# Kernel tuning notes

Measured on AMD Instinct MI355X. Metric: run time of the kernel, lower is better.

The kernel has to match this reference:

```python
import jax, jax.numpy as jnp
import numpy as np

B, T, D, H = 2, 2048, 1024, 16
DK = D // H


def setup_inputs() -> dict:
    key = jax.random.key(0)
    ks = jax.random.split(key, 9)
    x = jax.random.normal(ks[0], (B, T, D), dtype=jnp.float32)
    # causal mask, broadcastable to [B, H, T, T]; positions with 0 are masked
    mask = jnp.tril(jnp.ones((T, T), dtype=jnp.int32))[None, None]
    s = 1.0 / np.sqrt(D)
    Wq = jax.random.normal(ks[1], (D, D), dtype=jnp.float32) * s
    Wk = jax.random.normal(ks[2], (D, D), dtype=jnp.float32) * s
    Wv = jax.random.normal(ks[3], (D, D), dtype=jnp.float32) * s
    Wo = jax.random.normal(ks[4], (D, D), dtype=jnp.float32) * s
    bq = jnp.zeros((D,), jnp.float32)
    bk = jnp.zeros((D,), jnp.float32)
    bv = jnp.zeros((D,), jnp.float32)
    bo = jnp.zeros((D,), jnp.float32)
    return {"x": x, "mask": mask, "Wq": Wq, "bq": bq, "Wk": Wk, "bk": bk,
            "Wv": Wv, "bv": bv, "Wo": Wo, "bo": bo}


def _split_heads(t):
    # [B, T, D] -> [B, H, T, DK]
    return t.reshape(B, T, H, DK).transpose(0, 2, 1, 3)


def reference(x, mask, Wq, bq, Wk, bk, Wv, bv, Wo, bo):
    Q = _split_heads(x @ Wq.T + bq)
    K = _split_heads(x @ Wk.T + bk)
    V = _split_heads(x @ Wv.T + bv)
    scores = jnp.einsum('bhqd,bhkd->bhqk', Q, K) / jnp.sqrt(jnp.float32(DK))
    scores = jnp.where(mask == 0, jnp.float32(-1e9), scores)
    attn = jax.nn.softmax(scores, axis=-1)  # dropout p=0 -> identity
    out = jnp.einsum('bhqk,bhkd->bhqd', attn, V)
    out = out.transpose(0, 2, 1, 3).reshape(B, T, D)
    out = out @ Wo.T + bo
    return (out, attn)
```

## Files before the change

### kernel.cpp

```cpp
#include <hip/hip_runtime.h>
#include <hip/hip_bf16.h>
#include <cstdint>


typedef __attribute__((ext_vector_type(8))) short bf16x8;
typedef __attribute__((ext_vector_type(4))) float f32x4;

#define MFMA(a,b,c) __builtin_amdgcn_mfma_f32_16x16x32_bf16((a),(b),(c),0,0,0)

static __device__ __forceinline__ short f2bf(float f) {
  __hip_bfloat16 h = __float2bfloat16(f);
  return (short)__builtin_bit_cast(ushort, h);
}

static __device__ __forceinline__ bf16x8 cvt8(const float* p) {
  float4 v0 = *(const float4*)p;
  float4 v1 = *(const float4*)(p + 4);
  bf16x8 r;
  r[0] = f2bf(v0.x); r[1] = f2bf(v0.y); r[2] = f2bf(v0.z); r[3] = f2bf(v0.w);
  r[4] = f2bf(v1.x); r[5] = f2bf(v1.y); r[6] = f2bf(v1.z); r[7] = f2bf(v1.w);
  return r;
}

__global__ __launch_bounds__(256)
void cvt_x(const float* __restrict__ x, ushort* __restrict__ xbf)
{
  const size_t i = ((size_t)blockIdx.x * 256 + threadIdx.x) * 8;
  const bf16x8 v = cvt8(x + i);
  *(bf16x8*)&xbf[i] = v;
}

__global__ __launch_bounds__(256)
void gemm_qkv(const ushort* __restrict__ Xbf,
              const float* __restrict__ Wq, const float* __restrict__ Wk,
              const float* __restrict__ Wv,
              const float* __restrict__ bq, const float* __restrict__ bk,
              const float* __restrict__ bv,
              ushort* __restrict__ Qw, ushort* __restrict__ Kw, ushort* __restrict__ Vt)
{
  __shared__ __align__(16) ushort As[128 * 32];
  __shared__ __align__(16) ushort Bs[128 * 32];
  const int tid  = threadIdx.x;
  const int lane = tid & 63;
  const int wid  = tid >> 6;
  const int wr = wid >> 1, wc = wid & 1;
  const int g = lane >> 4, c16 = lane & 15;
  const int i0 = blockIdx.x * 128;
  const int j0 = blockIdx.y * 128;

  const int widx = j0 >> 10;
  const int jj0  = j0 & 1023;
  const float* W    = (widx == 0) ? Wq : ((widx == 1) ? Wk : Wv);
  const float* bias = (widx == 0) ? bq : ((widx == 1) ? bk : bv);

  const int arow = tid >> 2;
  const int acol = (tid & 3) * 8;
  const ushort* a0p = Xbf + (size_t)(i0 + arow) * 1024 + acol;
  const ushort* a1p = a0p + (size_t)64 * 1024;
  const float*  b0p = W + (size_t)(jj0 + arow) * 1024 + acol;
  const float*  b1p = b0p + (size_t)64 * 1024;

  f32x4 acc[4][4];
#pragma unroll
  for (int mi = 0; mi < 4; ++mi)
#pragma unroll
    for (int ni = 0; ni < 4; ++ni) acc[mi][ni] = (f32x4){0.f, 0.f, 0.f, 0.f};

  for (int k0 = 0; k0 < 1024; k0 += 32) {
    const bf16x8 va0 = *(const bf16x8*)(a0p + k0);
    const bf16x8 va1 = *(const bf16x8*)(a1p + k0);
    const bf16x8 vb0 = cvt8(b0p + k0);
    const bf16x8 vb1 = cvt8(b1p + k0);
    __syncthreads();
    *(bf16x8*)&As[tid * 8]        = va0;
    *(bf16x8*)&As[2048 + tid * 8] = va1;
    *(bf16x8*)&Bs[tid * 8]        = vb0;
    *(bf16x8*)&Bs[2048 + tid * 8] = vb1;
    __syncthreads();
    bf16x8 af[4], bfv[4];
#pragma unroll
    for (int mi = 0; mi < 4; ++mi)
      af[mi] = *(const bf16x8*)&As[(wr * 64 + mi * 16 + c16) * 32 + g * 8];
#pragma unroll
    for (int ni = 0; ni < 4; ++ni)
      bfv[ni] = *(const bf16x8*)&Bs[(wc * 64 + ni * 16 + c16) * 32 + g * 8];
#pragma unroll
    for (int mi = 0; mi < 4; ++mi)
#pragma unroll
      for (int ni = 0; ni < 4; ++ni)
        acc[mi][ni] = MFMA(af[mi], bfv[ni], acc[mi][ni]);
  }

  float bv4[4];
#pragma unroll
  for (int ni = 0; ni < 4; ++ni) bv4[ni] = bias[jj0 + wc * 64 + ni * 16 + c16];

  if (widx < 2) {
    ushort* OP = (widx == 0) ? Qw : Kw;
#pragma unroll
    for (int mi = 0; mi < 4; ++mi) {
      const int ib = i0 + wr * 64 + mi * 16 + g * 4;
      const int b = ib >> 11, t = ib & 2047;
#pragma unroll
      for (int ni = 0; ni < 4; ++ni) {
        const int jj = jj0 + wc * 64 + ni * 16 + c16;
        const int h = jj >> 6, dk = jj & 63;
        const size_t base = ((size_t)(b * 16 + h) * 2048 + t) * 64 + dk;
#pragma unroll
        for (int r = 0; r < 4; ++r)
          OP[base + (size_t)r * 64] = (ushort)f2bf(acc[mi][ni][r] + bv4[ni]);
      }
    }
  } else {
#pragma unroll
    for (int mi = 0; mi < 4; ++mi) {
      const int ib = i0 + wr * 64 + mi * 16 + g * 4;
      const int b = ib >> 11, t = ib & 2047;
#pragma unroll
      for (int ni = 0; ni < 4; ++ni) {
        const int jj = jj0 + wc * 64 + ni * 16 + c16;
        ushort4 pk;
        pk.x = (ushort)f2bf(acc[mi][ni][0] + bv4[ni]);
        pk.y = (ushort)f2bf(acc[mi][ni][1] + bv4[ni]);
        pk.z = (ushort)f2bf(acc[mi][ni][2] + bv4[ni]);
        pk.w = (ushort)f2bf(acc[mi][ni][3] + bv4[ni]);
        *(ushort4*)&Vt[((size_t)b * 1024 + jj) * 2048 + t] = pk;
      }
    }
  }
}

__global__ __launch_bounds__(256)
void gemm_out(const ushort* __restrict__ ctx, const float* __restrict__ Wo,
              const float* __restrict__ bo, float* __restrict__ out)
{
  __shared__ __align__(16) ushort As[128 * 32];
  __shared__ __align__(16) ushort Bs[128 * 32];
  const int tid  = threadIdx.x;
  const int lane = tid & 63;
  const int wid  = tid >> 6;
  const int wr = wid >> 1, wc = wid & 1;
  const int g = lane >> 4, c16 = lane & 15;
  const int i0 = blockIdx.x * 128;
  const int j0 = blockIdx.y * 128;

  const int arow = tid >> 2;
  const int acol = (tid & 3) * 8;
  const ushort* a0p = ctx + (size_t)(i0 + arow) * 1024 + acol;
  const ushort* a1p = a0p + (size_t)64 * 1024;
  const float*  b0p = Wo + (size_t)(j0 + arow) * 1024 + acol;
  const float*  b1p = b0p + (size_t)64 * 1024;

  f32x4 acc[4][4];
#pragma unroll
  for (int mi = 0; mi < 4; ++mi)
#pragma unroll
    for (int ni = 0; ni < 4; ++ni) acc[mi][ni] = (f32x4){0.f, 0.f, 0.f, 0.f};

  for (int k0 = 0; k0 < 1024; k0 += 32) {
    const bf16x8 va0 = *(const bf16x8*)(a0p + k0);
    const bf16x8 va1 = *(const bf16x8*)(a1p + k0);
    const bf16x8 vb0 = cvt8(b0p + k0);
    const bf16x8 vb1 = cvt8(b1p + k0);
    __syncthreads();
    *(bf16x8*)&As[tid * 8]        = va0;
    *(bf16x8*)&As[2048 + tid * 8] = va1;
    *(bf16x8*)&Bs[tid * 8]        = vb0;
    *(bf16x8*)&Bs[2048 + tid * 8] = vb1;
    __syncthreads();
    bf16x8 af[4], bfv[4];
#pragma unroll
    for (int mi = 0; mi < 4; ++mi)
      af[mi] = *(const bf16x8*)&As[(wr * 64 + mi * 16 + c16) * 32 + g * 8];
#pragma unroll
    for (int ni = 0; ni < 4; ++ni)
      bfv[ni] = *(const bf16x8*)&Bs[(wc * 64 + ni * 16 + c16) * 32 + g * 8];
#pragma unroll
    for (int mi = 0; mi < 4; ++mi)
#pragma unroll
      for (int ni = 0; ni < 4; ++ni)
        acc[mi][ni] = MFMA(af[mi], bfv[ni], acc[mi][ni]);
  }

  float bv4[4];
#pragma unroll
  for (int ni = 0; ni < 4; ++ni) bv4[ni] = bo[j0 + wc * 64 + ni * 16 + c16];

#pragma unroll
  for (int mi = 0; mi < 4; ++mi) {
    const int ib = i0 + wr * 64 + mi * 16 + g * 4;
#pragma unroll
    for (int ni = 0; ni < 4; ++ni) {
      const int jj = j0 + wc * 64 + ni * 16 + c16;
#pragma unroll
      for (int r = 0; r < 4; ++r)
        out[(size_t)(ib + r) * 1024 + jj] = acc[mi][ni][r] + bv4[ni];
    }
  }
}

__global__ __launch_bounds__(256)
void attn_stats(const ushort* __restrict__ Qw, const ushort* __restrict__ Kw,
                const ushort* __restrict__ Vt, ushort* __restrict__ ctx,
                float* __restrict__ Linv)
{
  __shared__ __align__(16) ushort Ks[2][64][68];
  __shared__ __align__(16) ushort Vs[2][64][68];
  __shared__ __align__(16) ushort Plds[4][16][68];
  const int tid = threadIdx.x, lane = tid & 63, wid = tid >> 6;
  const int g = lane >> 4, c16 = lane & 15;
  const int pr = blockIdx.x;
  const int bh = blockIdx.y;
  const int b = bh >> 4, h = bh & 15;

  const ushort* kbase = Kw + (size_t)bh * (2048 * 64);
  const ushort* vbase = Vt + ((size_t)b * 1024 + h * 64) * 2048;

  const int sr = tid >> 2;
  const int sc = (tid & 3) * 16;
  const ushort* kst = kbase + (size_t)sr * 64 + sc;
  const ushort* vst = vbase + (size_t)sr * 2048 + sc;

  int cur = 0;

#pragma unroll
  for (int part = 0; part < 2; ++part) {
    const int qtile = part ? (31 - pr) : pr;
    const int qt = qtile * 64 + wid * 16;
    const int q = qt + c16;
    const int nch = qtile + 1;

    const ushort* qp = Qw + ((size_t)bh * 2048 + q) * 64 + g * 8;
    const bf16x8 qf0 = *(const bf16x8*)qp;
    const bf16x8 qf1 = *(const bf16x8*)(qp + 32);

    f32x4 o[4];
#pragma unroll
    for (int dt = 0; dt < 4; ++dt) o[dt] = (f32x4){0.f, 0.f, 0.f, 0.f};
    float lsum = 0.f;

    {
      const bf16x8 k0 = *(const bf16x8*)kst;
      const bf16x8 k1 = *(const bf16x8*)(kst + 8);
      const bf16x8 v0 = *(const bf16x8*)vst;
      const bf16x8 v1 = *(const bf16x8*)(vst + 8);
      __syncthreads();
      *(bf16x8*)&Ks[cur][sr][sc]     = k0;
      *(bf16x8*)&Ks[cur][sr][sc + 8] = k1;
      *(bf16x8*)&Vs[cur][sr][sc]     = v0;
      *(bf16x8*)&Vs[cur][sr][sc + 8] = v1;
    }

    for (int c = 0; c < nch; ++c) {
      bf16x8 k0, k1, v0, v1;
      const bool pf = (c + 1 < nch);
      if (pf) {
        const int kt1 = (c + 1) * 64;
        k0 = *(const bf16x8*)(kst + (size_t)kt1 * 64);
        k1 = *(const bf16x8*)(kst + (size_t)kt1 * 64 + 8);
        v0 = *(const bf16x8*)(vst + kt1);
        v1 = *(const bf16x8*)(vst + kt1 + 8);
      }
      __syncthreads();

      const int kt = c * 64;
      f32x4 sv[4];
#pragma unroll
      for (int s = 0; s < 4; ++s) {
        const bf16x8 kf0 = *(const bf16x8*)&Ks[cur][s * 16 + c16][g * 8];
        const bf16x8 kf1 = *(const bf16x8*)&Ks[cur][s * 16 + c16][32 + g * 8];
        f32x4 t0 = (f32x4){0.f, 0.f, 0.f, 0.f};
        t0 = MFMA(kf0, qf0, t0);
        t0 = MFMA(kf1, qf1, t0);
        sv[s] = t0;
      }

      if (c + 1 == nch) {
#pragma unroll
        for (int s = 0; s < 4; ++s) {
          short pk[4];
#pragma unroll
          for (int r = 0; r < 4; ++r) {
            const int k = kt + s * 16 + g * 4 + r;
            const float p = (k > q) ? 0.f : __expf(sv[s][r] * 0.125f - 20.f);
            lsum += p;
            pk[r] = f2bf(p);
          }
          *(short4*)&Plds[wid][c16][s * 16 + g * 4] = *(short4*)pk;
        }
      } else {
#pragma unroll
        for (int s = 0; s < 4; ++s) {
          short pk[4];
#pragma unroll
          for (int r = 0; r < 4; ++r) {
            const float p = __expf(sv[s][r] * 0.125f - 20.f);
            lsum += p;
            pk[r] = f2bf(p);
          }
          *(short4*)&Plds[wid][c16][s * 16 + g * 4] = *(short4*)pk;
        }
      }

      {
        const bf16x8 pa0 = *(const bf16x8*)&Plds[wid][c16][g * 8];
#pragma unroll
        for (int dt = 0; dt < 4; ++dt) {
          const bf16x8 vf = *(const bf16x8*)&Vs[cur][dt * 16 + c16][g * 8];
          o[dt] = MFMA(pa0, vf, o[dt]);
        }
        const bf16x8 pa1 = *(const bf16x8*)&Plds[wid][c16][32 + g * 8];
#pragma unroll
        for (int dt = 0; dt < 4; ++dt) {
          const bf16x8 vf = *(const bf16x8*)&Vs[cur][dt * 16 + c16][32 + g * 8];
          o[dt] = MFMA(pa1, vf, o[dt]);
        }
      }

      if (pf) {
        *(bf16x8*)&Ks[cur ^ 1][sr][sc]     = k0;
        *(bf16x8*)&Ks[cur ^ 1][sr][sc + 8] = k1;
        *(bf16x8*)&Vs[cur ^ 1][sr][sc]     = v0;
        *(bf16x8*)&Vs[cur ^ 1][sr][sc + 8] = v1;
        cur ^= 1;
      }
    }

    lsum += __shfl_xor(lsum, 16);
    lsum += __shfl_xor(lsum, 32);
    const float linv = 1.f / lsum;
    if (g == 0) Linv[(size_t)bh * 2048 + q] = linv;

#pragma unroll
    for (int r = 0; r < 4; ++r) {
      const float lr = __shfl(linv, g * 4 + r);
#pragma unroll
      for (int dt = 0; dt < 4; ++dt)
        ctx[((size_t)(b * 2048 + qt + g * 4 + r)) * 1024 + h * 64 + dt * 16 + c16] =
            (ushort)f2bf(o[dt][r] * lr);
    }
  }
}

__global__ __launch_bounds__(256)
void attn_tiles(const ushort* __restrict__ Qw, const ushort* __restrict__ Kw,
                const float* __restrict__ Linv, float* __restrict__ attn)
{
  const int tid = threadIdx.x, lane = tid & 63, wid = tid >> 6;
  const int g = lane >> 4, c16 = lane & 15;
  const int bh = blockIdx.y;
  const int n = blockIdx.x * 4 + wid;
  int qtile = (int)((sqrtf(8.f * n + 1.f) - 1.f) * 0.5f);
  while ((qtile + 1) * (qtile + 2) / 2 <= n) ++qtile;
  while (qtile * (qtile + 1) / 2 > n) --qtile;
  const int ktile = n - qtile * (qtile + 1) / 2;
  const int qt0 = qtile * 64, kt0 = ktile * 64;
  float* abase = attn + ((size_t)bh * 2048) * 2048;

  const ushort* qbase = Qw + ((size_t)bh * 2048 + qt0) * 64;
  const ushort* kbase = Kw + ((size_t)bh * 2048 + kt0) * 64;
  bf16x8 qf0[4], qf1[4];
  float lv[4];
#pragma unroll
  for (int sq = 0; sq < 4; ++sq) {
    const ushort* qp = qbase + (size_t)(sq * 16 + c16) * 64 + g * 8;
    qf0[sq] = *(const bf16x8*)qp;
    qf1[sq] = *(const bf16x8*)(qp + 32);
    lv[sq] = Linv[(size_t)bh * 2048 + qt0 + sq * 16 + c16];
  }

  if (ktile < qtile) {
#pragma unroll
    for (int sk = 0; sk < 4; ++sk) {
      const ushort* kp = kbase + (size_t)(sk * 16 + c16) * 64 + g * 8;
      const bf16x8 kf0 = *(const bf16x8*)kp;
      const bf16x8 kf1 = *(const bf16x8*)(kp + 32);
#pragma unroll
      for (int sq = 0; sq < 4; ++sq) {
        f32x4 t = (f32x4){0.f, 0.f, 0.f, 0.f};
        t = MFMA(kf0, qf0[sq], t);
        t = MFMA(kf1, qf1[sq], t);
        const int qq = qt0 + sq * 16 + c16;
        f32x4 st;
#pragma unroll
        for (int r = 0; r < 4; ++r)
          st[r] = __expf(t[r] * 0.125f - 20.f) * lv[sq];
        __builtin_nontemporal_store(st,
            (f32x4*)(abase + (size_t)qq * 2048 + kt0 + sk * 16 + g * 4));
      }
    }
  } else {
#pragma unroll
    for (int sk = 0; sk < 4; ++sk) {
      const ushort* kp = kbase + (size_t)(sk * 16 + c16) * 64 + g * 8;
      const bf16x8 kf0 = *(const bf16x8*)kp;
      const bf16x8 kf1 = *(const bf16x8*)(kp + 32);
#pragma unroll
      for (int sq = 0; sq < 4; ++sq) {
        f32x4 t = (f32x4){0.f, 0.f, 0.f, 0.f};
        t = MFMA(kf0, qf0[sq], t);
        t = MFMA(kf1, qf1[sq], t);
        const int qq = qt0 + sq * 16 + c16;
        f32x4 st;
#pragma unroll
        for (int r = 0; r < 4; ++r) {
          const int kk = kt0 + sk * 16 + g * 4 + r;
          st[r] = (kk > qq) ? 0.f : __expf(t[r] * 0.125f - 20.f) * lv[sq];
        }
        __builtin_nontemporal_store(st,
            (f32x4*)(abase + (size_t)qq * 2048 + kt0 + sk * 16 + g * 4));
      }
    }
  }
}

__global__ __launch_bounds__(256)
void attn_zeros(float* __restrict__ attn)
{
  const int tid = threadIdx.x, lane = tid & 63, wid = tid >> 6;
  const int qtile = blockIdx.x;
  const int bh = blockIdx.y;
  const int zstart = (qtile + 1) * 64;
  const int zlen = 2048 - zstart;
  float* base = attn + ((size_t)bh * 2048 + qtile * 64) * 2048;
  const f32x4 z = (f32x4){0.f, 0.f, 0.f, 0.f};
#pragma unroll
  for (int rr = 0; rr < 16; ++rr) {
    float* rowp = base + (size_t)(wid * 16 + rr) * 2048 + zstart;
    for (int c = lane * 4; c < zlen; c += 256)
      __builtin_nontemporal_store(z, (f32x4*)(rowp + c));
  }
}

extern "C" void kernel_launch(void* const* d_in, const int* in_sizes, int n_in,
                              void* d_out, int out_size, void* d_ws, size_t ws_size,
                              hipStream_t stream)
{
  const float* x  = (const float*)d_in[0];
  const float* Wq = (const float*)d_in[2];
  const float* bq = (const float*)d_in[3];
  const float* Wk = (const float*)d_in[4];
  const float* bk = (const float*)d_in[5];
  const float* Wv = (const float*)d_in[6];
  const float* bv = (const float*)d_in[7];
  const float* Wo = (const float*)d_in[8];
  const float* bo = (const float*)d_in[9];

  if (ws_size < (size_t)33816576) return;

  float* out  = (float*)d_out;
  float* attn = out + (size_t)4194304;

  ushort* ws   = (ushort*)d_ws;
  ushort* Qw   = ws;
  ushort* Kw   = Qw + (size_t)4194304;
  ushort* Vtw  = Kw + (size_t)4194304;
  ushort* ctx  = Vtw + (size_t)4194304;
  float*  Linv = (float*)(ctx + (size_t)4194304);

  cvt_x<<<dim3(2048), 256, 0, stream>>>(x, ctx);
  gemm_qkv<<<dim3(32, 24), 256, 0, stream>>>(ctx, Wq, Wk, Wv, bq, bk, bv, Qw, Kw, Vtw);
  attn_stats<<<dim3(16, 32), 256, 0, stream>>>(Qw, Kw, Vtw, ctx, Linv);
  attn_zeros<<<dim3(31, 32), 256, 0, stream>>>(attn);
  attn_tiles<<<dim3(132, 32), 256, 0, stream>>>(Qw, Kw, Linv, attn);
  gemm_out<<<dim3(32, 8), 256, 0, stream>>>(ctx, Wo, bo, out);
}
```

Measured before the change: 272.3 us.

## Merge attention stats with zero-fill and attn tiles with output GEMM

Combines four launches into two by putting independent work into one grid. The attention-stats blocks and the upper-triangle zero-fill blocks share the first kernel. The probability-tile blocks and the output projection GEMM blocks share the second, each dispatched by blockIdx range. The aim is to cut launch overhead and let bandwidth-bound zero-fill and attn writes overlap with compute-bound work. The cost is heavier per-block register and LDS footprints, since each merged kernel takes the larger of its two roles, which may lower occupancy.

```diff
diff --git a/kernel.cpp b/kernel.cpp
--- a/kernel.cpp
+++ b/kernel.cpp
@@ -131,18 +131,250 @@
 }
 
 __global__ __launch_bounds__(256)
-void gemm_out(const ushort* __restrict__ ctx, const float* __restrict__ Wo,
-              const float* __restrict__ bo, float* __restrict__ out)
+void stats_zeros(const ushort* __restrict__ Qw, const ushort* __restrict__ Kw,
+                 const ushort* __restrict__ Vt, ushort* __restrict__ ctx,
+                 float* __restrict__ Linv, float* __restrict__ attn)
+{
+  __shared__ __align__(16) ushort Ks[2][64][68];
+  __shared__ __align__(16) ushort Vs[2][64][68];
+  __shared__ __align__(16) ushort Plds[4][16][68];
+  const int tid = threadIdx.x, lane = tid & 63, wid = tid >> 6;
+
+  if (blockIdx.x >= 512) {
+    const int zi = blockIdx.x - 512;
+    const int qtile = zi % 31;
+    const int bh = zi / 31;
+    const int zstart = (qtile + 1) * 64;
+    const int zlen = 2048 - zstart;
+    float* base = attn + ((size_t)bh * 2048 + qtile * 64) * 2048;
+    const f32x4 z = (f32x4){0.f, 0.f, 0.f, 0.f};
+#pragma unroll
+    for (int rr = 0; rr < 16; ++rr) {
+      float* rowp = base + (size_t)(wid * 16 + rr) * 2048 + zstart;
+      for (int c = lane * 4; c < zlen; c += 256)
+        __builtin_nontemporal_store(z, (f32x4*)(rowp + c));
+    }
+    return;
+  }
+
+  const int g = lane >> 4, c16 = lane & 15;
+  const int pr = blockIdx.x & 15;
+  const int bh = blockIdx.x >> 4;
+  const int b = bh >> 4, h = bh & 15;
+
+  const ushort* kbase = Kw + (size_t)bh * (2048 * 64);
+  const ushort* vbase = Vt + ((size_t)b * 1024 + h * 64) * 2048;
+
+  const int sr = tid >> 2;
+  const int sc = (tid & 3) * 16;
+  const ushort* kst = kbase + (size_t)sr * 64 + sc;
+  const ushort* vst = vbase + (size_t)sr * 2048 + sc;
+
+  int cur = 0;
+
+#pragma unroll
+  for (int part = 0; part < 2; ++part) {
+    const int qtile = part ? (31 - pr) : pr;
+    const int qt = qtile * 64 + wid * 16;
+    const int q = qt + c16;
+    const int nch = qtile + 1;
+
+    const ushort* qp = Qw + ((size_t)bh * 2048 + q) * 64 + g * 8;
+    const bf16x8 qf0 = *(const bf16x8*)qp;
+    const bf16x8 qf1 = *(const bf16x8*)(qp + 32);
+
+    f32x4 o[4];
+#pragma unroll
+    for (int dt = 0; dt < 4; ++dt) o[dt] = (f32x4){0.f, 0.f, 0.f, 0.f};
+    float lsum = 0.f;
+
+    {
+      const bf16x8 k0 = *(const bf16x8*)kst;
+      const bf16x8 k1 = *(const bf16x8*)(kst + 8);
+      const bf16x8 v0 = *(const bf16x8*)vst;
+      const bf16x8 v1 = *(const bf16x8*)(vst + 8);
+      __syncthreads();
+      *(bf16x8*)&Ks[cur][sr][sc]     = k0;
+      *(bf16x8*)&Ks[cur][sr][sc + 8] = k1;
+      *(bf16x8*)&Vs[cur][sr][sc]     = v0;
+      *(bf16x8*)&Vs[cur][sr][sc + 8] = v1;
+    }
+
+    for (int c = 0; c < nch; ++c) {
+      bf16x8 k0, k1, v0, v1;
+      const bool pf = (c + 1 < nch);
+      if (pf) {
+        const int kt1 = (c + 1) * 64;
+        k0 = *(const bf16x8*)(kst + (size_t)kt1 * 64);
+        k1 = *(const bf16x8*)(kst + (size_t)kt1 * 64 + 8);
+        v0 = *(const bf16x8*)(vst + kt1);
+        v1 = *(const bf16x8*)(vst + kt1 + 8);
+      }
+      __syncthreads();
+
+      const int kt = c * 64;
+      f32x4 sv[4];
+#pragma unroll
+      for (int s = 0; s < 4; ++s) {
+        const bf16x8 kf0 = *(const bf16x8*)&Ks[cur][s * 16 + c16][g * 8];
+        const bf16x8 kf1 = *(const bf16x8*)&Ks[cur][s * 16 + c16][32 + g * 8];
+        f32x4 t0 = (f32x4){0.f, 0.f, 0.f, 0.f};
+        t0 = MFMA(kf0, qf0, t0);
+        t0 = MFMA(kf1, qf1, t0);
+        sv[s] = t0;
+      }
+
+      if (c + 1 == nch) {
+#pragma unroll
+        for (int s = 0; s < 4; ++s) {
+          short pk[4];
+#pragma unroll
+          for (int r = 0; r < 4; ++r) {
+            const int k = kt + s * 16 + g * 4 + r;
+            const float p = (k > q) ? 0.f : __expf(sv[s][r] * 0.125f - 20.f);
+            lsum += p;
+            pk[r] = f2bf(p);
+          }
+          *(short4*)&Plds[wid][c16][s * 16 + g * 4] = *(short4*)pk;
+        }
+      } else {
+#pragma unroll
+        for (int s = 0; s < 4; ++s) {
+          short pk[4];
+#pragma unroll
+          for (int r = 0; r < 4; ++r) {
+            const float p = __expf(sv[s][r] * 0.125f - 20.f);
+            lsum += p;
+            pk[r] = f2bf(p);
+          }
+          *(short4*)&Plds[wid][c16][s * 16 + g * 4] = *(short4*)pk;
+        }
+      }
+
+      {
+        const bf16x8 pa0 = *(const bf16x8*)&Plds[wid][c16][g * 8];
+#pragma unroll
+        for (int dt = 0; dt < 4; ++dt) {
+          const bf16x8 vf = *(const bf16x8*)&Vs[cur][dt * 16 + c16][g * 8];
+          o[dt] = MFMA(pa0, vf, o[dt]);
+        }
+        const bf16x8 pa1 = *(const bf16x8*)&Plds[wid][c16][32 + g * 8];
+#pragma unroll
+        for (int dt = 0; dt < 4; ++dt) {
+          const bf16x8 vf = *(const bf16x8*)&Vs[cur][dt * 16 + c16][32 + g * 8];
+          o[dt] = MFMA(pa1, vf, o[dt]);
+        }
+      }
+
+      if (pf) {
+        *(bf16x8*)&Ks[cur ^ 1][sr][sc]     = k0;
+        *(bf16x8*)&Ks[cur ^ 1][sr][sc + 8] = k1;
+        *(bf16x8*)&Vs[cur ^ 1][sr][sc]     = v0;
+        *(bf16x8*)&Vs[cur ^ 1][sr][sc + 8] = v1;
+        cur ^= 1;
+      }
+    }
+
+    lsum += __shfl_xor(lsum, 16);
+    lsum += __shfl_xor(lsum, 32);
+    const float linv = 1.f / lsum;
+    if (g == 0) Linv[(size_t)bh * 2048 + q] = linv;
+
+#pragma unroll
+    for (int r = 0; r < 4; ++r) {
+      const float lr = __shfl(linv, g * 4 + r);
+#pragma unroll
+      for (int dt = 0; dt < 4; ++dt)
+        ctx[((size_t)(b * 2048 + qt + g * 4 + r)) * 1024 + h * 64 + dt * 16 + c16] =
+            (ushort)f2bf(o[dt][r] * lr);
+    }
+  }
+}
+
+__global__ __launch_bounds__(256)
+void tiles_out(const ushort* __restrict__ Qw, const ushort* __restrict__ Kw,
+               const float* __restrict__ Linv, float* __restrict__ attn,
+               const ushort* __restrict__ ctx, const float* __restrict__ Wo,
+               const float* __restrict__ bo, float* __restrict__ out)
 {
   __shared__ __align__(16) ushort As[128 * 32];
   __shared__ __align__(16) ushort Bs[128 * 32];
-  const int tid  = threadIdx.x;
-  const int lane = tid & 63;
-  const int wid  = tid >> 6;
+  const int tid = threadIdx.x, lane = tid & 63, wid = tid >> 6;
+  const int g = lane >> 4, c16 = lane & 15;
+
+  if (blockIdx.x < 4224) {
+    const int bx = blockIdx.x % 132;
+    const int bh = blockIdx.x / 132;
+    const int n = bx * 4 + wid;
+    int qtile = (int)((sqrtf(8.f * n + 1.f) - 1.f) * 0.5f);
+    while ((qtile + 1) * (qtile + 2) / 2 <= n) ++qtile;
+    while (qtile * (qtile + 1) / 2 > n) --qtile;
+    const int ktile = n - qtile * (qtile + 1) / 2;
+    const int qt0 = qtile * 64, kt0 = ktile * 64;
+    float* abase = attn + ((size_t)bh * 2048) * 2048;
+
+    const ushort* qbase = Qw + ((size_t)bh * 2048 + qt0) * 64;
+    const ushort* kbase = Kw + ((size_t)bh * 2048 + kt0) * 64;
+    bf16x8 qf0[4], qf1[4];
+    float lv[4];
+#pragma unroll
+    for (int sq = 0; sq < 4; ++sq) {
+      const ushort* qp = qbase + (size_t)(sq * 16 + c16) * 64 + g * 8;
+      qf0[sq] = *(const bf16x8*)qp;
+      qf1[sq] = *(const bf16x8*)(qp + 32);
+      lv[sq] = Linv[(size_t)bh * 2048 + qt0 + sq * 16 + c16];
+    }
+
+    if (ktile < qtile) {
+#pragma unroll
+      for (int sk = 0; sk < 4; ++sk) {
+        const ushort* kp = kbase + (size_t)(sk * 16 + c16) * 64 + g * 8;
+        const bf16x8 kf0 = *(const bf16x8*)kp;
+        const bf16x8 kf1 = *(const bf16x8*)(kp + 32);
+#pragma unroll
+        for (int sq = 0; sq < 4; ++sq) {
+          f32x4 t = (f32x4){0.f, 0.f, 0.f, 0.f};
+          t = MFMA(kf0, qf0[sq], t);
+          t = MFMA(kf1, qf1[sq], t);
+          const int qq = qt0 + sq * 16 + c16;
+          f32x4 st;
+#pragma unroll
+          for (int r = 0; r < 4; ++r)
+            st[r] = __expf(t[r] * 0.125f - 20.f) * lv[sq];
+          __builtin_nontemporal_store(st,
+              (f32x4*)(abase + (size_t)qq * 2048 + kt0 + sk * 16 + g * 4));
+        }
+      }
+    } else {
+#pragma unroll
+      for (int sk = 0; sk < 4; ++sk) {
+        const ushort* kp = kbase + (size_t)(sk * 16 + c16) * 64 + g * 8;
+        const bf16x8 kf0 = *(const bf16x8*)kp;
+        const bf16x8 kf1 = *(const bf16x8*)(kp + 32);
+#pragma unroll
+        for (int sq = 0; sq < 4; ++sq) {
+          f32x4 t = (f32x4){0.f, 0.f, 0.f, 0.f};
+          t = MFMA(kf0, qf0[sq], t);
+          t = MFMA(kf1, qf1[sq], t);
+          const int qq = qt0 + sq * 16 + c16;
+          f32x4 st;
+#pragma unroll
+          for (int r = 0; r < 4; ++r) {
+            const int kk = kt0 + sk * 16 + g * 4 + r;
+            st[r] = (kk > qq) ? 0.f : __expf(t[r] * 0.125f - 20.f) * lv[sq];
+          }
+          __builtin_nontemporal_store(st,
+              (f32x4*)(abase + (size_t)qq * 2048 + kt0 + sk * 16 + g * 4));
+        }
+      }
+    }
+    return;
+  }
+
+  const int j = blockIdx.x - 4224;
   const int wr = wid >> 1, wc = wid & 1;
-  const int g = lane >> 4, c16 = lane & 15;
-  const int i0 = blockIdx.x * 128;
-  const int j0 = blockIdx.y * 128;
+  const int i0 = (j & 31) * 128;
+  const int j0 = (j >> 5) * 128;
 
   const int arow = tid >> 2;
   const int acol = (tid & 3) * 8;
@@ -196,239 +428,6 @@
       for (int r = 0; r < 4; ++r)
         out[(size_t)(ib + r) * 1024 + jj] = acc[mi][ni][r] + bv4[ni];
     }
-  }
-}
-
-__global__ __launch_bounds__(256)
-void attn_stats(const ushort* __restrict__ Qw, const ushort* __restrict__ Kw,
-                const ushort* __restrict__ Vt, ushort* __restrict__ ctx,
-                float* __restrict__ Linv)
-{
-  __shared__ __align__(16) ushort Ks[2][64][68];
-  __shared__ __align__(16) ushort Vs[2][64][68];
-  __shared__ __align__(16) ushort Plds[4][16][68];
-  const int tid = threadIdx.x, lane = tid & 63, wid = tid >> 6;
-  const int g = lane >> 4, c16 = lane & 15;
-  const int pr = blockIdx.x;
-  const int bh = blockIdx.y;
-  const int b = bh >> 4, h = bh & 15;
-
-  const ushort* kbase = Kw + (size_t)bh * (2048 * 64);
-  const ushort* vbase = Vt + ((size_t)b * 1024 + h * 64) * 2048;
-
-  const int sr = tid >> 2;
-  const int sc = (tid & 3) * 16;
-  const ushort* kst = kbase + (size_t)sr * 64 + sc;
-  const ushort* vst = vbase + (size_t)sr * 2048 + sc;
-
-  int cur = 0;
-
-#pragma unroll
-  for (int part = 0; part < 2; ++part) {
-    const int qtile = part ? (31 - pr) : pr;
-    const int qt = qtile * 64 + wid * 16;
-    const int q = qt + c16;
-    const int nch = qtile + 1;
-
-    const ushort* qp = Qw + ((size_t)bh * 2048 + q) * 64 + g * 8;
-    const bf16x8 qf0 = *(const bf16x8*)qp;
-    const bf16x8 qf1 = *(const bf16x8*)(qp + 32);
-
-    f32x4 o[4];
-#pragma unroll
-    for (int dt = 0; dt < 4; ++dt) o[dt] = (f32x4){0.f, 0.f, 0.f, 0.f};
-    float lsum = 0.f;
-
-    {
-      const bf16x8 k0 = *(const bf16x8*)kst;
-      const bf16x8 k1 = *(const bf16x8*)(kst + 8);
-      const bf16x8 v0 = *(const bf16x8*)vst;
-      const bf16x8 v1 = *(const bf16x8*)(vst + 8);
-      __syncthreads();
-      *(bf16x8*)&Ks[cur][sr][sc]     = k0;
-      *(bf16x8*)&Ks[cur][sr][sc + 8] = k1;
-      *(bf16x8*)&Vs[cur][sr][sc]     = v0;
-      *(bf16x8*)&Vs[cur][sr][sc + 8] = v1;
-    }
-
-    for (int c = 0; c < nch; ++c) {
-      bf16x8 k0, k1, v0, v1;
-      const bool pf = (c + 1 < nch);
-      if (pf) {
-        const int kt1 = (c + 1) * 64;
-        k0 = *(const bf16x8*)(kst + (size_t)kt1 * 64);
-        k1 = *(const bf16x8*)(kst + (size_t)kt1 * 64 + 8);
-        v0 = *(const bf16x8*)(vst + kt1);
-        v1 = *(const bf16x8*)(vst + kt1 + 8);
-      }
-      __syncthreads();
-
-      const int kt = c * 64;
-      f32x4 sv[4];
-#pragma unroll
-      for (int s = 0; s < 4; ++s) {
-        const bf16x8 kf0 = *(const bf16x8*)&Ks[cur][s * 16 + c16][g * 8];
-        const bf16x8 kf1 = *(const bf16x8*)&Ks[cur][s * 16 + c16][32 + g * 8];
-        f32x4 t0 = (f32x4){0.f, 0.f, 0.f, 0.f};
-        t0 = MFMA(kf0, qf0, t0);
-        t0 = MFMA(kf1, qf1, t0);
-        sv[s] = t0;
-      }
-
-      if (c + 1 == nch) {
-#pragma unroll
-        for (int s = 0; s < 4; ++s) {
-          short pk[4];
-#pragma unroll
-          for (int r = 0; r < 4; ++r) {
-            const int k = kt + s * 16 + g * 4 + r;
-            const float p = (k > q) ? 0.f : __expf(sv[s][r] * 0.125f - 20.f);
-            lsum += p;
-            pk[r] = f2bf(p);
-          }
-          *(short4*)&Plds[wid][c16][s * 16 + g * 4] = *(short4*)pk;
-        }
-      } else {
-#pragma unroll
-        for (int s = 0; s < 4; ++s) {
-          short pk[4];
-#pragma unroll
-          for (int r = 0; r < 4; ++r) {
-            const float p = __expf(sv[s][r] * 0.125f - 20.f);
-            lsum += p;
-            pk[r] = f2bf(p);
-          }
-          *(short4*)&Plds[wid][c16][s * 16 + g * 4] = *(short4*)pk;
-        }
-      }
-
-      {
-        const bf16x8 pa0 = *(const bf16x8*)&Plds[wid][c16][g * 8];
-#pragma unroll
-        for (int dt = 0; dt < 4; ++dt) {
-          const bf16x8 vf = *(const bf16x8*)&Vs[cur][dt * 16 + c16][g * 8];
-          o[dt] = MFMA(pa0, vf, o[dt]);
-        }
-        const bf16x8 pa1 = *(const bf16x8*)&Plds[wid][c16][32 + g * 8];
-#pragma unroll
-        for (int dt = 0; dt < 4; ++dt) {
-          const bf16x8 vf = *(const bf16x8*)&Vs[cur][dt * 16 + c16][32 + g * 8];
-          o[dt] = MFMA(pa1, vf, o[dt]);
-        }
-      }
-
-      if (pf) {
-        *(bf16x8*)&Ks[cur ^ 1][sr][sc]     = k0;
-        *(bf16x8*)&Ks[cur ^ 1][sr][sc + 8] = k1;
-        *(bf16x8*)&Vs[cur ^ 1][sr][sc]     = v0;
-        *(bf16x8*)&Vs[cur ^ 1][sr][sc + 8] = v1;
-        cur ^= 1;
-      }
-    }
-
-    lsum += __shfl_xor(lsum, 16);
-    lsum += __shfl_xor(lsum, 32);
-    const float linv = 1.f / lsum;
-    if (g == 0) Linv[(size_t)bh * 2048 + q] = linv;
-
-#pragma unroll
-    for (int r = 0; r < 4; ++r) {
-      const float lr = __shfl(linv, g * 4 + r);
-#pragma unroll
-      for (int dt = 0; dt < 4; ++dt)
-        ctx[((size_t)(b * 2048 + qt + g * 4 + r)) * 1024 + h * 64 + dt * 16 + c16] =
-            (ushort)f2bf(o[dt][r] * lr);
-    }
-  }
-}
-
-__global__ __launch_bounds__(256)
-void attn_tiles(const ushort* __restrict__ Qw, const ushort* __restrict__ Kw,
-                const float* __restrict__ Linv, float* __restrict__ attn)
-{
-  const int tid = threadIdx.x, lane = tid & 63, wid = tid >> 6;
-  const int g = lane >> 4, c16 = lane & 15;
-  const int bh = blockIdx.y;
-  const int n = blockIdx.x * 4 + wid;
-  int qtile = (int)((sqrtf(8.f * n + 1.f) - 1.f) * 0.5f);
-  while ((qtile + 1) * (qtile + 2) / 2 <= n) ++qtile;
-  while (qtile * (qtile + 1) / 2 > n) --qtile;
-  const int ktile = n - qtile * (qtile + 1) / 2;
-  const int qt0 = qtile * 64, kt0 = ktile * 64;
-  float* abase = attn + ((size_t)bh * 2048) * 2048;
-
-  const ushort* qbase = Qw + ((size_t)bh * 2048 + qt0) * 64;
-  const ushort* kbase = Kw + ((size_t)bh * 2048 + kt0) * 64;
-  bf16x8 qf0[4], qf1[4];
-  float lv[4];
-#pragma unroll
-  for (int sq = 0; sq < 4; ++sq) {
-    const ushort* qp = qbase + (size_t)(sq * 16 + c16) * 64 + g * 8;
-    qf0[sq] = *(const bf16x8*)qp;
-    qf1[sq] = *(const bf16x8*)(qp + 32);
-    lv[sq] = Linv[(size_t)bh * 2048 + qt0 + sq * 16 + c16];
-  }
-
-  if (ktile < qtile) {
-#pragma unroll
-    for (int sk = 0; sk < 4; ++sk) {
-      const ushort* kp = kbase + (size_t)(sk * 16 + c16) * 64 + g * 8;
-      const bf16x8 kf0 = *(const bf16x8*)kp;
-      const bf16x8 kf1 = *(const bf16x8*)(kp + 32);
-#pragma unroll
-      for (int sq = 0; sq < 4; ++sq) {
-        f32x4 t = (f32x4){0.f, 0.f, 0.f, 0.f};
-        t = MFMA(kf0, qf0[sq], t);
-        t = MFMA(kf1, qf1[sq], t);
-        const int qq = qt0 + sq * 16 + c16;
-        f32x4 st;
-#pragma unroll
-        for (int r = 0; r < 4; ++r)
-          st[r] = __expf(t[r] * 0.125f - 20.f) * lv[sq];
-        __builtin_nontemporal_store(st,
-            (f32x4*)(abase + (size_t)qq * 2048 + kt0 + sk * 16 + g * 4));
-      }
-    }
-  } else {
-#pragma unroll
-    for (int sk = 0; sk < 4; ++sk) {
-      const ushort* kp = kbase + (size_t)(sk * 16 + c16) * 64 + g * 8;
-      const bf16x8 kf0 = *(const bf16x8*)kp;
-      const bf16x8 kf1 = *(const bf16x8*)(kp + 32);
-#pragma unroll
-      for (int sq = 0; sq < 4; ++sq) {
-        f32x4 t = (f32x4){0.f, 0.f, 0.f, 0.f};
-        t = MFMA(kf0, qf0[sq], t);
-        t = MFMA(kf1, qf1[sq], t);
-        const int qq = qt0 + sq * 16 + c16;
-        f32x4 st;
-#pragma unroll
-        for (int r = 0; r < 4; ++r) {
-          const int kk = kt0 + sk * 16 + g * 4 + r;
-          st[r] = (kk > qq) ? 0.f : __expf(t[r] * 0.125f - 20.f) * lv[sq];
-        }
-        __builtin_nontemporal_store(st,
-            (f32x4*)(abase + (size_t)qq * 2048 + kt0 + sk * 16 + g * 4));
-      }
-    }
-  }
-}
-
-__global__ __launch_bounds__(256)
-void attn_zeros(float* __restrict__ attn)
-{
-  const int tid = threadIdx.x, lane = tid & 63, wid = tid >> 6;
-  const int qtile = blockIdx.x;
-  const int bh = blockIdx.y;
-  const int zstart = (qtile + 1) * 64;
-  const int zlen = 2048 - zstart;
-  float* base = attn + ((size_t)bh * 2048 + qtile * 64) * 2048;
-  const f32x4 z = (f32x4){0.f, 0.f, 0.f, 0.f};
-#pragma unroll
-  for (int rr = 0; rr < 16; ++rr) {
-    float* rowp = base + (size_t)(wid * 16 + rr) * 2048 + zstart;
-    for (int c = lane * 4; c < zlen; c += 256)
-      __builtin_nontemporal_store(z, (f32x4*)(rowp + c));
   }
 }
 
@@ -460,8 +459,6 @@
 
   cvt_x<<<dim3(2048), 256, 0, stream>>>(x, ctx);
   gemm_qkv<<<dim3(32, 24), 256, 0, stream>>>(ctx, Wq, Wk, Wv, bq, bk, bv, Qw, Kw, Vtw);
-  attn_stats<<<dim3(16, 32), 256, 0, stream>>>(Qw, Kw, Vtw, ctx, Linv);
-  attn_zeros<<<dim3(31, 32), 256, 0, stream>>>(attn);
-  attn_tiles<<<dim3(132, 32), 256, 0, stream>>>(Qw, Kw, Linv, attn);
-  gemm_out<<<dim3(32, 8), 256, 0, stream>>>(ctx, Wo, bo, out);
-}
+  stats_zeros<<<dim3(1504), 256, 0, stream>>>(Qw, Kw, Vtw, ctx, Linv, attn);
+  tiles_out<<<dim3(4480), 256, 0, stream>>>(Qw, Kw, Linv, attn, ctx, Wo, bo, out);
+}
```

After: 236.1 us. 13.3% less time.
